# Kernel optimization log

Measured on AMD Instinct MI355X. Metric: run time of the kernel, lower is better.

Reference implementation:

```python
import jax, jax.numpy as jnp
import numpy as np

NODE_TO_JOINT = [-1, 0, 1, 2, 3, 4, 5, 6, 7, 8, 9, 10, 11]
EMBED_DIM = 256
DIM_PER_OUT = 2
NUM_JOINTS = max(j for j in NODE_TO_JOINT if j >= 0) + 1
# node index that produces each joint, in ascending joint order
JOINT_TO_NODE = np.full(NUM_JOINTS, -1, dtype=np.int32)
for node_idx, joint_idx in enumerate(NODE_TO_JOINT):
    if joint_idx >= 0:
        JOINT_TO_NODE[joint_idx] = node_idx


def setup_inputs() -> dict:
    key = jax.random.key(0)
    kx, kw, kb = jax.random.split(key, 3)
    B = 65536
    x = jax.random.normal(kx, (B, len(NODE_TO_JOINT), EMBED_DIM), dtype=jnp.float32)
    # per-joint Linear heads stacked: W [J, D, K], b [J, K] (Kaiming-uniform-ish init)
    bound = 1.0 / np.sqrt(EMBED_DIM)
    W = jax.random.uniform(kw, (NUM_JOINTS, EMBED_DIM, DIM_PER_OUT), minval=-bound, maxval=bound, dtype=jnp.float32)
    b = jax.random.uniform(kb, (NUM_JOINTS, DIM_PER_OUT), minval=-bound, maxval=bound, dtype=jnp.float32)
    return {"x": x, "W": W, "b": b}


def reference(x, W, b):
    # x: [B, N, D]; gather actuated-node embeddings in joint order -> [B, J, D]
    xg = x[:, jnp.asarray(JOINT_TO_NODE), :]
    # fused batched per-joint linear: [B, J, K]
    out = jnp.einsum('bjd,jdk->bjk', xg, W) + b
    return out
```

## Files before the change

### kernel.cpp

```cpp
#include <hip/hip_runtime.h>


#define WAVE 64

__global__ __launch_bounds__(256) void detok_kernel(
    const float* __restrict__ x, const float* __restrict__ W,
    const float* __restrict__ bias, float* __restrict__ out,
    int total_pairs)
{
    const int lane = (int)(threadIdx.x & 63u);
    const int waves_per_block = (int)(blockDim.x >> 6);
    const int wave_in_block = (int)(threadIdx.x >> 6);
    int wave_id = (int)blockIdx.x * waves_per_block + wave_in_block;
    const int num_waves = (int)gridDim.x * waves_per_block;

    for (int p = wave_id; p < total_pairs; p += num_waves) {
        const int b = p / 12;
        const int j = p - b * 12;

        const float4* xp =
            (const float4*)(x + ((size_t)(b * 13 + j + 1)) * 256) + lane;
        const float4 xv = *xp;

        const float4* wp = (const float4*)(W + (size_t)j * 512 + (size_t)lane * 8);
        const float4 w0 = wp[0];
        const float4 w1 = wp[1];

        float s0 = xv.x * w0.x + xv.y * w0.z + xv.z * w1.x + xv.w * w1.z;
        float s1 = xv.x * w0.y + xv.y * w0.w + xv.z * w1.y + xv.w * w1.w;

        #pragma unroll
        for (int off = 32; off > 0; off >>= 1) {
            s0 += __shfl_xor(s0, off, WAVE);
            s1 += __shfl_xor(s1, off, WAVE);
        }

        if (lane == 0) {
            float2 r;
            r.x = s0 + bias[j * 2 + 0];
            r.y = s1 + bias[j * 2 + 1];
            *(float2*)(out + (size_t)p * 2) = r;
        }
    }
}

extern "C" void kernel_launch(void* const* d_in, const int* in_sizes, int n_in,
                              void* d_out, int out_size, void* d_ws, size_t ws_size,
                              hipStream_t stream) {
    const float* x    = (const float*)d_in[0];
    const float* W    = (const float*)d_in[1];
    const float* bias = (const float*)d_in[2];
    float* out        = (float*)d_out;

    const int B = in_sizes[0] / (13 * 256);
    const int total_pairs = B * 12;

    const int blocks = 4096;
    detok_kernel<<<blocks, 256, 0, stream>>>(x, W, bias, out, total_pairs);
}
```

Measured before the change: 1.105 ms.

## Process sixteen joint rows per wave with four lanes per row

Each wavefront now handles 16 (batch, joint) pairs at once, with each group of four lanes striding across a row in a 16-iteration loop, instead of one pair per wave followed by a full 64-lane shuffle reduction. This cuts the reduction from six shuffle steps to two and raises per-thread work and memory-level parallelism. The grid is enlarged to 12288 blocks. Each lane's loads become strided 16-byte accesses per row rather than fully contiguous wave-wide reads, which may hurt coalescing, and the pair count must be divisible by 16.

```diff
diff --git a/kernel.cpp b/kernel.cpp
--- a/kernel.cpp
+++ b/kernel.cpp
@@ -1,41 +1,42 @@
 #include <hip/hip_runtime.h>
 
-
-#define WAVE 64
 
 __global__ __launch_bounds__(256) void detok_kernel(
     const float* __restrict__ x, const float* __restrict__ W,
     const float* __restrict__ bias, float* __restrict__ out,
-    int total_pairs)
+    int num_batches)
 {
     const int lane = (int)(threadIdx.x & 63u);
-    const int waves_per_block = (int)(blockDim.x >> 6);
-    const int wave_in_block = (int)(threadIdx.x >> 6);
-    int wave_id = (int)blockIdx.x * waves_per_block + wave_in_block;
-    const int num_waves = (int)gridDim.x * waves_per_block;
+    const int g = lane >> 2;
+    const int q = lane & 3;
 
-    for (int p = wave_id; p < total_pairs; p += num_waves) {
+    const int wave_id = (int)blockIdx.x * ((int)blockDim.x >> 6) + ((int)threadIdx.x >> 6);
+    const int num_waves = (int)gridDim.x * ((int)blockDim.x >> 6);
+
+    for (int batch = wave_id; batch < num_batches; batch += num_waves) {
+        const int p = (batch << 4) + g;
         const int b = p / 12;
         const int j = p - b * 12;
 
-        const float4* xp =
-            (const float4*)(x + ((size_t)(b * 13 + j + 1)) * 256) + lane;
-        const float4 xv = *xp;
+        const float* xrow = x + (size_t)(b * 13 + j + 1) * 256 + q * 4;
+        const float* wrow = W + (size_t)j * 512 + q * 8;
 
-        const float4* wp = (const float4*)(W + (size_t)j * 512 + (size_t)lane * 8);
-        const float4 w0 = wp[0];
-        const float4 w1 = wp[1];
-
-        float s0 = xv.x * w0.x + xv.y * w0.z + xv.z * w1.x + xv.w * w1.z;
-        float s1 = xv.x * w0.y + xv.y * w0.w + xv.z * w1.y + xv.w * w1.w;
-
+        float s0 = 0.f, s1 = 0.f;
         #pragma unroll
-        for (int off = 32; off > 0; off >>= 1) {
-            s0 += __shfl_xor(s0, off, WAVE);
-            s1 += __shfl_xor(s1, off, WAVE);
+        for (int i = 0; i < 16; ++i) {
+            const float4 xv = *(const float4*)(xrow + i * 16);
+            const float4 w0 = *(const float4*)(wrow + i * 32);
+            const float4 w1 = *(const float4*)(wrow + i * 32 + 4);
+            s0 += xv.x * w0.x + xv.y * w0.z + xv.z * w1.x + xv.w * w1.z;
+            s1 += xv.x * w0.y + xv.y * w0.w + xv.z * w1.y + xv.w * w1.w;
         }
 
-        if (lane == 0) {
+        s0 += __shfl_xor(s0, 1, 64);
+        s1 += __shfl_xor(s1, 1, 64);
+        s0 += __shfl_xor(s0, 2, 64);
+        s1 += __shfl_xor(s1, 2, 64);
+
+        if (q == 0) {
             float2 r;
             r.x = s0 + bias[j * 2 + 0];
             r.y = s1 + bias[j * 2 + 1];
@@ -54,7 +55,8 @@
 
     const int B = in_sizes[0] / (13 * 256);
     const int total_pairs = B * 12;
+    const int num_batches = total_pairs >> 4;
 
-    const int blocks = 4096;
-    detok_kernel<<<blocks, 256, 0, stream>>>(x, W, bias, out, total_pairs);
+    const int blocks = 12288;
+    detok_kernel<<<blocks, 256, 0, stream>>>(x, W, bias, out, num_batches);
 }
```

Result: no change. 1.094 ms (-1.0%).
